# Kernel tuning notes

Measured on AMD Instinct MI355X. Metric: run time of the kernel, lower is better.

Reference implementation:

```python
import jax, jax.numpy as jnp
from jax import lax
import numpy as np

T, B, NIN = 512, 512, 64
H1, H2, H3 = 100, 50, 25


def lstm_layer(x, w_ih, w_hh, b_ih, b_hh):
    # x: [T, B, in]; torch gate order (i, f, g, o); weights [4H, in]/[4H, H]
    H = w_hh.shape[1]
    xg = jnp.einsum('tbi,gi->tbg', x, w_ih) + b_ih + b_hh  # [T, B, 4H]

    def step(carry, xg_t):
        h, c = carry
        g = xg_t + h @ w_hh.T
        i, f, gg, o = jnp.split(g, 4, axis=-1)
        c = jax.nn.sigmoid(f) * c + jax.nn.sigmoid(i) * jnp.tanh(gg)
        h = jax.nn.sigmoid(o) * jnp.tanh(c)
        return (h, c), h

    h0 = jnp.zeros((x.shape[1], H), x.dtype)
    _, hs = lax.scan(step, (h0, h0), xg)
    return hs  # [T, B, H]


def setup_inputs() -> dict:
    key = jax.random.key(0)
    ks = jax.random.split(key, 16)
    s = 0.1  # init scale for stability
    return {
        'x': jax.random.normal(ks[0], (T, B, NIN), jnp.float32),
        'w_ih1': jax.random.normal(ks[1], (4 * H1, NIN), jnp.float32) * s,
        'w_hh1': jax.random.normal(ks[2], (4 * H1, H1), jnp.float32) * s,
        'b_ih1': jax.random.normal(ks[3], (4 * H1,), jnp.float32) * s,
        'b_hh1': jax.random.normal(ks[4], (4 * H1,), jnp.float32) * s,
        'w_ih2': jax.random.normal(ks[5], (4 * H2, H1), jnp.float32) * s,
        'w_hh2': jax.random.normal(ks[6], (4 * H2, H2), jnp.float32) * s,
        'b_ih2': jax.random.normal(ks[7], (4 * H2,), jnp.float32) * s,
        'b_hh2': jax.random.normal(ks[8], (4 * H2,), jnp.float32) * s,
        'w_ih3': jax.random.normal(ks[9], (4 * H3, H2), jnp.float32) * s,
        'w_hh3': jax.random.normal(ks[10], (4 * H3, H3), jnp.float32) * s,
        'b_ih3': jax.random.normal(ks[11], (4 * H3,), jnp.float32) * s,
        'b_hh3': jax.random.normal(ks[12], (4 * H3,), jnp.float32) * s,
        'w_lin': jax.random.normal(ks[13], (1, H3), jnp.float32) * s,
        'b_lin': jax.random.normal(ks[14], (1,), jnp.float32) * s,
    }


def reference(x, w_ih1, w_hh1, b_ih1, b_hh1,
              w_ih2, w_hh2, b_ih2, b_hh2,
              w_ih3, w_hh3, b_ih3, b_hh3,
              w_lin, b_lin):
    # Dropout layers are identity at inference.
    h = lstm_layer(x, w_ih1, w_hh1, b_ih1, b_hh1)
    h = lstm_layer(h, w_ih2, w_hh2, b_ih2, b_hh2)
    h = lstm_layer(h, w_ih3, w_hh3, b_ih3, b_hh3)
    return h @ w_lin.T + b_lin  # [T, B, 1]
```

## Files before the change

### kernel.cpp

```cpp
#include <hip/hip_runtime.h>
#include <math.h>

#define T_STEPS 512
#define BATCH   512

__device__ __forceinline__ float sigmoidf_(float x) {
    return 1.0f / (1.0f + __expf(-x));
}
__device__ __forceinline__ float tanhf_(float x) {
    float ax = fabsf(x);
    float e  = __expf(-2.0f * ax);
    float t  = (1.0f - e) / (1.0f + e);
    return copysignf(t, x);
}
__device__ __forceinline__ float4 ld4(const float* p) {
    return make_float4(p[0], p[1], p[2], p[3]);
}

#define PINF(f)  asm volatile("" : "+v"(f))
#define PIN4(v)  { PINF(v.x); PINF(v.y); PINF(v.z); PINF(v.w); }

__global__ __launch_bounds__(448, 2) void gemm1_kernel(
    const float* __restrict__ A, const float* __restrict__ W,
    const float* __restrict__ bih, const float* __restrict__ bhh,
    float* __restrict__ xg)
{
    __shared__ __align__(16) float As[64 * 64];
    const int tid = threadIdx.x;

    float4 W00,W01,W02,W03,W04,W05,W06,W07,W08,W09,W10,W11,W12,W13,W14,W15;
    float bias = 0.0f;
    if (tid < 400) {
        bias = bih[tid] + bhh[tid];
        const float* wp = W + tid * 64;
        W00=ld4(wp+ 0); W01=ld4(wp+ 4); W02=ld4(wp+ 8); W03=ld4(wp+12);
        W04=ld4(wp+16); W05=ld4(wp+20); W06=ld4(wp+24); W07=ld4(wp+28);
        W08=ld4(wp+32); W09=ld4(wp+36); W10=ld4(wp+40); W11=ld4(wp+44);
        W12=ld4(wp+48); W13=ld4(wp+52); W14=ld4(wp+56); W15=ld4(wp+60);
        PIN4(W00) PIN4(W01) PIN4(W02) PIN4(W03)
        PIN4(W04) PIN4(W05) PIN4(W06) PIN4(W07)
        PIN4(W08) PIN4(W09) PIN4(W10) PIN4(W11)
        PIN4(W12) PIN4(W13) PIN4(W14) PIN4(W15)
        PINF(bias);
    }

    const size_t r0 = (size_t)blockIdx.x * 64;
    const float4* Ag = (const float4*)(A + r0 * 64);
    float4* As4 = (float4*)As;
    for (int i = tid; i < 64 * 16; i += 448) As4[i] = Ag[i];
    __syncthreads();

    if (tid < 400) {
        for (int r = 0; r < 64; ++r) {
            const float4* a4 = (const float4*)(As + r * 64);
            float a0 = bias, a1 = 0.0f;
#define G1V(WV, I) { float4 v = a4[I]; \
            a0 = fmaf(v.x, WV.x, a0); a1 = fmaf(v.y, WV.y, a1); \
            a0 = fmaf(v.z, WV.z, a0); a1 = fmaf(v.w, WV.w, a1); }
            G1V(W00,0) G1V(W01,1) G1V(W02,2) G1V(W03,3)
            G1V(W04,4) G1V(W05,5) G1V(W06,6) G1V(W07,7)
            G1V(W08,8) G1V(W09,9) G1V(W10,10) G1V(W11,11)
            G1V(W12,12) G1V(W13,13) G1V(W14,14) G1V(W15,15)
#undef G1V
            xg[(r0 + r) * 400 + tid] = a0 + a1;
        }
    }
}

__global__ __launch_bounds__(448, 2) void gemm2_kernel(
    const float* __restrict__ A,
    const float* __restrict__ W,
    const float* __restrict__ bih, const float* __restrict__ bhh,
    float* __restrict__ xg)
{
    __shared__ __align__(16) float As[64 * 104];
    __shared__ __align__(16) float ps[8][2][200];

    const int tid  = threadIdx.x;
    const bool slot = (tid < 400);
    const int q = slot ? tid / 200 : 0;
    const int j = slot ? tid % 200 : 0;

    float4 W00,W01,W02,W03,W04,W05,W06,W07,W08,W09,W10,W11,W12;
    float bias = 0.0f;
    if (slot) {
        if (q == 0) bias = bih[j] + bhh[j];
        const float* wp = W + j * 100 + q * 52;
        W00=ld4(wp+ 0); W01=ld4(wp+ 4); W02=ld4(wp+ 8); W03=ld4(wp+12);
        W04=ld4(wp+16); W05=ld4(wp+20); W06=ld4(wp+24); W07=ld4(wp+28);
        W08=ld4(wp+32); W09=ld4(wp+36); W10=ld4(wp+40); W11=ld4(wp+44);
        W12 = q ? make_float4(0.f,0.f,0.f,0.f) : ld4(wp+48);
        PIN4(W00) PIN4(W01) PIN4(W02) PIN4(W03)
        PIN4(W04) PIN4(W05) PIN4(W06) PIN4(W07)
        PIN4(W08) PIN4(W09) PIN4(W10) PIN4(W11)
        PIN4(W12)
        PINF(bias);
    }

    const size_t r0 = (size_t)blockIdx.x * 64;
    const float2* A2 = (const float2*)(A + r0 * 100);
    float2* As2 = (float2*)As;
    for (int i = tid; i < 64 * 50; i += 448) {
        int r = i / 50, k2 = i % 50;
        As2[r * 52 + k2] = A2[i];
    }
    if (tid < 64) {
        As[tid*104+100]=0.f; As[tid*104+101]=0.f;
        As[tid*104+102]=0.f; As[tid*104+103]=0.f;
    }
    __syncthreads();

    const float4* As4 = (const float4*)As;
    const int q13 = q * 13;
    const float base = (q == 0) ? bias : 0.0f;
    for (int g = 0; g < 8; ++g) {
        const int rb = g * 8;
        if (slot) {
#define G2V(P, WV, I) { float4 v = P[I]; \
            A0 = fmaf(v.x, WV.x, A0); A1 = fmaf(v.y, WV.y, A1); \
            A0 = fmaf(v.z, WV.z, A0); A1 = fmaf(v.w, WV.w, A1); }
#define G2ROW(RR) { const float4* a4 = As4 + (rb + RR) * 26 + q13; \
            float A0 = base, A1 = 0.0f; \
            G2V(a4,W00,0) G2V(a4,W01,1) G2V(a4,W02,2) G2V(a4,W03,3) \
            G2V(a4,W04,4) G2V(a4,W05,5) G2V(a4,W06,6) G2V(a4,W07,7) \
            G2V(a4,W08,8) G2V(a4,W09,9) G2V(a4,W10,10) G2V(a4,W11,11) \
            G2V(a4,W12,12) \
            ps[RR][q][j] = A0 + A1; }
            G2ROW(0) G2ROW(1) G2ROW(2) G2ROW(3)
            G2ROW(4) G2ROW(5) G2ROW(6) G2ROW(7)
#undef G2ROW
#undef G2V
        }
        __syncthreads();
        if (tid < 200) {
            #pragma unroll
            for (int rr = 0; rr < 8; ++rr)
                xg[(r0 + rb + rr) * 200 + tid] = ps[rr][0][tid] + ps[rr][1][tid];
        }
        __syncthreads();
    }
}

__global__ __launch_bounds__(832, 3) void scan1_kernel(
    const float* __restrict__ xg,
    const float* __restrict__ w_hh,
    float* __restrict__ h1c,
    float* __restrict__ c1state,
    int t0, int CH)
{
    __shared__ __align__(16) float h_s[2][104];
    __shared__ __align__(16) float ps[2][2][400];

    const int tid   = threadIdx.x;
    const int q     = (tid >= 416) ? 1 : 0;
    const int j     = tid - 416 * q;
    const bool slot = (j < 400);
    const int brow0 = blockIdx.x * 2;

    float4 W00,W01,W02,W03,W04,W05,W06,W07,W08,W09,W10,W11,W12;
    if (slot) {
        const float* wp = w_hh + j * 100 + q * 52;
        W00=ld4(wp+ 0); W01=ld4(wp+ 4); W02=ld4(wp+ 8); W03=ld4(wp+12);
        W04=ld4(wp+16); W05=ld4(wp+20); W06=ld4(wp+24); W07=ld4(wp+28);
        W08=ld4(wp+32); W09=ld4(wp+36); W10=ld4(wp+40); W11=ld4(wp+44);
        W12 = q ? make_float4(0.f,0.f,0.f,0.f) : ld4(wp+48);
        PIN4(W00) PIN4(W01) PIN4(W02) PIN4(W03)
        PIN4(W04) PIN4(W05) PIN4(W06) PIN4(W07)
        PIN4(W08) PIN4(W09) PIN4(W10) PIN4(W11)
        PIN4(W12)
    }

    float c = 0.0f;
    if (tid < 200) {
        int bn = tid / 100, u = tid % 100;
        if (t0 == 0) {
            h_s[bn][u] = 0.0f;
        } else {
            h_s[bn][u] = h1c[((size_t)(CH - 1) * BATCH + brow0 + bn) * 100 + u];
            c          = c1state[(size_t)(brow0 + bn) * 100 + u];
        }
    }
    if (tid >= 200 && tid < 208) {
        int i = tid - 200;
        h_s[i >> 2][100 + (i & 3)] = 0.0f;
    }

    float xgv0 = 0.0f, xgv1 = 0.0f;
    if (slot && q == 0) {
        xgv0 = xg[(size_t)brow0 * 400 + j];
        xgv1 = xg[((size_t)brow0 + 1) * 400 + j];
    }
    __syncthreads();

    const int hq = q * 13;
    for (int tl = 0; tl < CH; ++tl) {
        float pre0 = 0.0f, pre1 = 0.0f;
        if (slot && q == 0 && tl + 1 < CH) {
            pre0 = xg[((size_t)(tl + 1) * BATCH + brow0) * 400 + j];
            pre1 = xg[((size_t)(tl + 1) * BATCH + brow0 + 1) * 400 + j];
        }
        if (slot) {
            const float4* h0 = (const float4*)h_s[0] + hq;
            const float4* h1 = (const float4*)h_s[1] + hq;
            float a00 = xgv0, a01 = 0.0f, a10 = xgv1, a11 = 0.0f;
#define S1ACC(WV, I) { float4 v0 = h0[I], v1 = h1[I]; \
            a00 = fmaf(v0.x, WV.x, a00); a10 = fmaf(v1.x, WV.x, a10); \
            a01 = fmaf(v0.y, WV.y, a01); a11 = fmaf(v1.y, WV.y, a11); \
            a00 = fmaf(v0.z, WV.z, a00); a10 = fmaf(v1.z, WV.z, a10); \
            a01 = fmaf(v0.w, WV.w, a01); a11 = fmaf(v1.w, WV.w, a11); }
            S1ACC(W00,0) S1ACC(W01,1) S1ACC(W02,2) S1ACC(W03,3)
            S1ACC(W04,4) S1ACC(W05,5) S1ACC(W06,6) S1ACC(W07,7)
            S1ACC(W08,8) S1ACC(W09,9) S1ACC(W10,10) S1ACC(W11,11)
            S1ACC(W12,12)
#undef S1ACC
            ps[0][q][j] = a00 + a01;
            ps[1][q][j] = a10 + a11;
        }
        __syncthreads();
        xgv0 = pre0; xgv1 = pre1;
        if (tid < 200) {
            int bn = tid / 100, u = tid % 100;
            float gi = ps[bn][0][u]       + ps[bn][1][u];
            float gf = ps[bn][0][100 + u] + ps[bn][1][100 + u];
            float gg = ps[bn][0][200 + u] + ps[bn][1][200 + u];
            float go = ps[bn][0][300 + u] + ps[bn][1][300 + u];
            c = sigmoidf_(gf) * c + sigmoidf_(gi) * tanhf_(gg);
            float h = sigmoidf_(go) * tanhf_(c);
            h_s[bn][u] = h;
            h1c[((size_t)tl * BATCH + brow0 + bn) * 100 + u] = h;
        }
        __syncthreads();
    }
    if (tid < 200) {
        int bn = tid / 100, u = tid % 100;
        c1state[(size_t)(brow0 + bn) * 100 + u] = c;
    }
}

__global__ __launch_bounds__(384, 2) void scan23_kernel(
    const float* __restrict__ xg2,
    const float* __restrict__ w_hh2,
    const float* __restrict__ w_ih3,
    const float* __restrict__ w_hh3,
    const float* __restrict__ b_ih3, const float* __restrict__ b_hh3,
    const float* __restrict__ w_lin, const float* __restrict__ b_lin,
    float* __restrict__ out,
    float* __restrict__ h2state, float* __restrict__ c2state,
    float* __restrict__ h3state, float* __restrict__ c3state,
    int t0, int CH)
{
    __shared__ __align__(16) float h2_s[52];
    __shared__ __align__(16) float x3_s[2][52];
    __shared__ __align__(16) float h3_s[28];
    __shared__ __align__(16) float h3o_s[2][28];
    __shared__ __align__(16) float g2_s[200];
    __shared__ __align__(16) float g3_s[100];

    const int tid  = threadIdx.x;
    const int brow = blockIdx.x;

    float4 WA0,WA1,WA2,WA3,WA4,WA5,WA6,WA7,WA8,WA9,WA10,WA11,WA12;
    float4 WB0,WB1,WB2,WB3,WB4,WB5,WB6;
    float bias = 0.0f;

#define PINA13 { PIN4(WA0) PIN4(WA1) PIN4(WA2) PIN4(WA3) PIN4(WA4) PIN4(WA5) \
                 PIN4(WA6) PIN4(WA7) PIN4(WA8) PIN4(WA9) PIN4(WA10) PIN4(WA11) \
                 PIN4(WA12) }
#define PINB7  { PIN4(WB0) PIN4(WB1) PIN4(WB2) PIN4(WB3) PIN4(WB4) PIN4(WB5) \
                 PIN4(WB6) }

    if (tid < 200) {
        const float* p = w_hh2 + tid * 50;
        WA0=ld4(p+ 0); WA1=ld4(p+ 4); WA2=ld4(p+ 8); WA3=ld4(p+12);
        WA4=ld4(p+16); WA5=ld4(p+20); WA6=ld4(p+24); WA7=ld4(p+28);
        WA8=ld4(p+32); WA9=ld4(p+36); WA10=ld4(p+40); WA11=ld4(p+44);
        WA12 = make_float4(p[48], p[49], 0.f, 0.f);
        PINA13
    } else if (tid >= 256 && tid < 356) {
        int jj = tid - 256;
        bias = b_ih3[jj] + b_hh3[jj];
        const float* p = w_ih3 + jj * 50;
        WA0=ld4(p+ 0); WA1=ld4(p+ 4); WA2=ld4(p+ 8); WA3=ld4(p+12);
        WA4=ld4(p+16); WA5=ld4(p+20); WA6=ld4(p+24); WA7=ld4(p+28);
        WA8=ld4(p+32); WA9=ld4(p+36); WA10=ld4(p+40); WA11=ld4(p+44);
        WA12 = make_float4(p[48], p[49], 0.f, 0.f);
        const float* p2 = w_hh3 + jj * 25;
        WB0=ld4(p2+ 0); WB1=ld4(p2+ 4); WB2=ld4(p2+ 8);
        WB3=ld4(p2+12); WB4=ld4(p2+16); WB5=ld4(p2+20);
        WB6 = make_float4(p2[24], 0.f, 0.f, 0.f);
        PINA13
        PINB7
        PINF(bias);
    } else if (tid == 370) {
        bias = b_lin[0];
        WA0=ld4(w_lin+ 0); WA1=ld4(w_lin+ 4); WA2=ld4(w_lin+ 8);
        WA3=ld4(w_lin+12); WA4=ld4(w_lin+16); WA5=ld4(w_lin+20);
        WA6 = make_float4(w_lin[24], 0.f, 0.f, 0.f);
        PIN4(WA0) PIN4(WA1) PIN4(WA2) PIN4(WA3) PIN4(WA4) PIN4(WA5) PIN4(WA6)
        PINF(bias);
    }
#undef PINA13
#undef PINB7

    float c2 = 0.0f, c3 = 0.0f;
    if (tid < 52)  { h2_s[tid] = 0.0f; x3_s[0][tid] = 0.0f; x3_s[1][tid] = 0.0f; }
    if (tid >= 52 && tid < 80)  h3_s[tid - 52] = 0.0f;
    if (tid >= 80 && tid < 108) h3o_s[0][tid - 80] = 0.0f;
    if (tid >= 108 && tid < 136) h3o_s[1][tid - 108] = 0.0f;
    __syncthreads();
    if (t0 > 0) {
        if (tid < 50) {
            h2_s[tid] = h2state[(size_t)brow * 50 + tid];
            c2        = c2state[(size_t)brow * 50 + tid];
        }
        if (tid >= 256 && tid < 281) {
            int u = tid - 256;
            h3_s[u] = h3state[(size_t)brow * 25 + u];
            c3      = c3state[(size_t)brow * 25 + u];
        }
    }
    float xgv = (tid < 200) ? xg2[(size_t)brow * 200 + tid] : 0.0f;
    __syncthreads();

    for (int it = 0; it < CH + 2; ++it) {
        float pre = (tid < 200 && it + 1 < CH)
                  ? xg2[((size_t)(it + 1) * BATCH + brow) * 200 + tid] : 0.0f;

        if (tid < 200 && it < CH) {
            const float4* hv = (const float4*)h2_s;
            float a0 = xgv, a1 = 0.0f;
#define SCV(PV, WV, I) { float4 v = PV[I]; \
            a0 = fmaf(v.x, WV.x, a0); a1 = fmaf(v.y, WV.y, a1); \
            a0 = fmaf(v.z, WV.z, a0); a1 = fmaf(v.w, WV.w, a1); }
            SCV(hv,WA0,0) SCV(hv,WA1,1) SCV(hv,WA2,2) SCV(hv,WA3,3)
            SCV(hv,WA4,4) SCV(hv,WA5,5) SCV(hv,WA6,6) SCV(hv,WA7,7)
            SCV(hv,WA8,8) SCV(hv,WA9,9) SCV(hv,WA10,10) SCV(hv,WA11,11)
            SCV(hv,WA12,12)
            g2_s[tid] = a0 + a1;
        }

        if (tid >= 256 && tid < 356 && it >= 1 && it <= CH) {
            const float4* xv = (const float4*)x3_s[(it - 1) & 1];
            const float4* hv = (const float4*)h3_s;
            float a0 = bias, a1 = 0.0f;
            SCV(xv,WA0,0) SCV(xv,WA1,1) SCV(xv,WA2,2) SCV(xv,WA3,3)
            SCV(xv,WA4,4) SCV(xv,WA5,5) SCV(xv,WA6,6) SCV(xv,WA7,7)
            SCV(xv,WA8,8) SCV(xv,WA9,9) SCV(xv,WA10,10) SCV(xv,WA11,11)
            SCV(xv,WA12,12)
            SCV(hv,WB0,0) SCV(hv,WB1,1) SCV(hv,WB2,2) SCV(hv,WB3,3)
            SCV(hv,WB4,4) SCV(hv,WB5,5) SCV(hv,WB6,6)
            g3_s[tid - 256] = a0 + a1;
        }

        if (tid == 370 && it >= 2) {
            const float4* hv = (const float4*)h3o_s[(it - 2) & 1];
            float a0 = bias, a1 = 0.0f;
            SCV(hv,WA0,0) SCV(hv,WA1,1) SCV(hv,WA2,2) SCV(hv,WA3,3)
            SCV(hv,WA4,4) SCV(hv,WA5,5) SCV(hv,WA6,6)
            out[(size_t)(t0 + it - 2) * BATCH + brow] = a0 + a1;
        }
#undef SCV
        __syncthreads();

        if (tid < 200) xgv = pre;

        if (tid < 50 && it < CH) {
            float gi = g2_s[tid],       gf = g2_s[50 + tid];
            float gg = g2_s[100 + tid], go = g2_s[150 + tid];
            c2 = sigmoidf_(gf) * c2 + sigmoidf_(gi) * tanhf_(gg);
            float h = sigmoidf_(go) * tanhf_(c2);
            h2_s[tid] = h;
            x3_s[it & 1][tid] = h;
        }

        if (tid >= 256 && tid < 281 && it >= 1 && it <= CH) {
            int u = tid - 256;
            float gi = g3_s[u],      gf = g3_s[25 + u];
            float gg = g3_s[50 + u], go = g3_s[75 + u];
            c3 = sigmoidf_(gf) * c3 + sigmoidf_(gi) * tanhf_(gg);
            float h = sigmoidf_(go) * tanhf_(c3);
            h3_s[u] = h;
            h3o_s[(it - 1) & 1][u] = h;
        }
        __syncthreads();
    }

    if (tid < 50) {
        h2state[(size_t)brow * 50 + tid] = h2_s[tid];
        c2state[(size_t)brow * 50 + tid] = c2;
    }
    if (tid >= 256 && tid < 281) {
        int u = tid - 256;
        h3state[(size_t)brow * 25 + u] = h3_s[u];
        c3state[(size_t)brow * 25 + u] = c3;
    }
}

extern "C" void kernel_launch(void* const* d_in, const int* in_sizes, int n_in,
                              void* d_out, int out_size, void* d_ws, size_t ws_size,
                              hipStream_t stream)
{
    const float* x     = (const float*)d_in[0];
    const float* w_ih1 = (const float*)d_in[1];
    const float* w_hh1 = (const float*)d_in[2];
    const float* b_ih1 = (const float*)d_in[3];
    const float* b_hh1 = (const float*)d_in[4];
    const float* w_ih2 = (const float*)d_in[5];
    const float* w_hh2 = (const float*)d_in[6];
    const float* b_ih2 = (const float*)d_in[7];
    const float* b_hh2 = (const float*)d_in[8];
    const float* w_ih3 = (const float*)d_in[9];
    const float* w_hh3 = (const float*)d_in[10];
    const float* b_ih3 = (const float*)d_in[11];
    const float* b_hh3 = (const float*)d_in[12];
    const float* w_lin = (const float*)d_in[13];
    const float* b_lin = (const float*)d_in[14];
    float* out = (float*)d_out;

    const size_t state_bytes = (size_t)BATCH * (100 + 50 + 50 + 25 + 25) * sizeof(float);
    int CH = 0;
    for (int c = 128; c >= 8; c >>= 1) {
        size_t need = (size_t)c * BATCH * 700 * sizeof(float) + state_bytes;
        if (need <= ws_size) { CH = c; break; }
    }
    if (CH == 0) return;

    char* ws = (char*)d_ws;
    float* xg1c    = (float*)ws;
    float* h1c     = xg1c + (size_t)CH * BATCH * 400;
    float* xg2c    = h1c  + (size_t)CH * BATCH * 100;
    float* c1state = xg2c + (size_t)CH * BATCH * 200;
    float* h2state = c1state + (size_t)BATCH * 100;
    float* c2state = h2state + (size_t)BATCH * 50;
    float* h3state = c2state + (size_t)BATCH * 50;
    float* c3state = h3state + (size_t)BATCH * 25;

    const int rowtiles = CH * BATCH / 64;

    for (int t0 = 0; t0 < T_STEPS; t0 += CH) {
        gemm1_kernel<<<rowtiles, 448, 0, stream>>>(
            x + (size_t)t0 * BATCH * 64, w_ih1, b_ih1, b_hh1, xg1c);
        scan1_kernel<<<BATCH / 2, 832, 0, stream>>>(xg1c, w_hh1, h1c, c1state, t0, CH);
        gemm2_kernel<<<rowtiles, 448, 0, stream>>>(h1c, w_ih2, b_ih2, b_hh2, xg2c);
        scan23_kernel<<<BATCH, 384, 0, stream>>>(
            xg2c, w_hh2, w_ih3, w_hh3, b_ih3, b_hh3, w_lin, b_lin, out,
            h2state, c2state, h3state, c3state, t0, CH);
    }
}
```

Measured before the change: 1.916 ms.

## Stage layer-1 recurrent weights in LDS and compute all four gates per thread

The layer-1 scan kernel stops holding w_hh in registers split across 832 threads. It now copies the full 400x100 weight matrix into about 160 KB of dynamic LDS, transposed, and each of 200 active threads computes all four gates for one hidden unit of one batch row. This removes the partial-sum exchange through shared memory and the cross-thread gate gather. The cost is reading weights from LDS on every step, staging 160 KB per block, and only one block per CU. The register-pinning asm barriers in the two GEMM kernels are also removed.

```diff
diff --git a/kernel.cpp b/kernel.cpp
--- a/kernel.cpp
+++ b/kernel.cpp
@@ -37,11 +37,6 @@
         W04=ld4(wp+16); W05=ld4(wp+20); W06=ld4(wp+24); W07=ld4(wp+28);
         W08=ld4(wp+32); W09=ld4(wp+36); W10=ld4(wp+40); W11=ld4(wp+44);
         W12=ld4(wp+48); W13=ld4(wp+52); W14=ld4(wp+56); W15=ld4(wp+60);
-        PIN4(W00) PIN4(W01) PIN4(W02) PIN4(W03)
-        PIN4(W04) PIN4(W05) PIN4(W06) PIN4(W07)
-        PIN4(W08) PIN4(W09) PIN4(W10) PIN4(W11)
-        PIN4(W12) PIN4(W13) PIN4(W14) PIN4(W15)
-        PINF(bias);
     }
 
     const size_t r0 = (size_t)blockIdx.x * 64;
@@ -68,8 +63,7 @@
 }
 
 __global__ __launch_bounds__(448, 2) void gemm2_kernel(
-    const float* __restrict__ A,
-    const float* __restrict__ W,
+    const float* __restrict__ A, const float* __restrict__ W,
     const float* __restrict__ bih, const float* __restrict__ bhh,
     float* __restrict__ xg)
 {
@@ -90,11 +84,6 @@
         W04=ld4(wp+16); W05=ld4(wp+20); W06=ld4(wp+24); W07=ld4(wp+28);
         W08=ld4(wp+32); W09=ld4(wp+36); W10=ld4(wp+40); W11=ld4(wp+44);
         W12 = q ? make_float4(0.f,0.f,0.f,0.f) : ld4(wp+48);
-        PIN4(W00) PIN4(W01) PIN4(W02) PIN4(W03)
-        PIN4(W04) PIN4(W05) PIN4(W06) PIN4(W07)
-        PIN4(W08) PIN4(W09) PIN4(W10) PIN4(W11)
-        PIN4(W12)
-        PINF(bias);
     }
 
     const size_t r0 = (size_t)blockIdx.x * 64;
@@ -141,100 +130,85 @@
     }
 }
 
-__global__ __launch_bounds__(832, 3) void scan1_kernel(
+__global__ __launch_bounds__(256, 1) void scan1_kernel(
     const float* __restrict__ xg,
     const float* __restrict__ w_hh,
     float* __restrict__ h1c,
     float* __restrict__ c1state,
     int t0, int CH)
 {
-    __shared__ __align__(16) float h_s[2][104];
-    __shared__ __align__(16) float ps[2][2][400];
-
-    const int tid   = threadIdx.x;
-    const int q     = (tid >= 416) ? 1 : 0;
-    const int j     = tid - 416 * q;
-    const bool slot = (j < 400);
+    extern __shared__ __align__(16) char smem[];
+    float4* wt = (float4*)smem;
+    float* hA = (float*)(smem + 160000);
+    float* hB = (float*)(smem + 160400);
+
+    const int tid = threadIdx.x;
     const int brow0 = blockIdx.x * 2;
 
-    float4 W00,W01,W02,W03,W04,W05,W06,W07,W08,W09,W10,W11,W12;
-    if (slot) {
-        const float* wp = w_hh + j * 100 + q * 52;
-        W00=ld4(wp+ 0); W01=ld4(wp+ 4); W02=ld4(wp+ 8); W03=ld4(wp+12);
-        W04=ld4(wp+16); W05=ld4(wp+20); W06=ld4(wp+24); W07=ld4(wp+28);
-        W08=ld4(wp+32); W09=ld4(wp+36); W10=ld4(wp+40); W11=ld4(wp+44);
-        W12 = q ? make_float4(0.f,0.f,0.f,0.f) : ld4(wp+48);
-        PIN4(W00) PIN4(W01) PIN4(W02) PIN4(W03)
-        PIN4(W04) PIN4(W05) PIN4(W06) PIN4(W07)
-        PIN4(W08) PIN4(W09) PIN4(W10) PIN4(W11)
-        PIN4(W12)
-    }
+    for (int e = tid; e < 10000; e += 256) {
+        int j = e % 400, m = e / 400;
+        wt[m * 400 + j] = *(const float4*)(w_hh + j * 100 + 4 * m);
+    }
+
+    const bool act = (tid < 200);
+    const int u = tid >> 1;
+    const int r = tid & 1;
+    const int row = brow0 + r;
 
     float c = 0.0f;
-    if (tid < 200) {
-        int bn = tid / 100, u = tid % 100;
-        if (t0 == 0) {
-            h_s[bn][u] = 0.0f;
-        } else {
-            h_s[bn][u] = h1c[((size_t)(CH - 1) * BATCH + brow0 + bn) * 100 + u];
-            c          = c1state[(size_t)(brow0 + bn) * 100 + u];
-        }
-    }
-    if (tid >= 200 && tid < 208) {
-        int i = tid - 200;
-        h_s[i >> 2][100 + (i & 3)] = 0.0f;
-    }
-
-    float xgv0 = 0.0f, xgv1 = 0.0f;
-    if (slot && q == 0) {
-        xgv0 = xg[(size_t)brow0 * 400 + j];
-        xgv1 = xg[((size_t)brow0 + 1) * 400 + j];
+    if (act) {
+        float h0 = 0.0f;
+        if (t0 > 0) {
+            h0 = h1c[((size_t)(CH - 1) * BATCH + row) * 100 + u];
+            c  = c1state[(size_t)row * 100 + u];
+        }
+        (r ? hB : hA)[u] = h0;
+    }
+    float xI = 0.f, xF = 0.f, xG = 0.f, xO = 0.f;
+    if (act) {
+        const float* xp = xg + (size_t)row * 400 + u;
+        xI = xp[0]; xF = xp[100]; xG = xp[200]; xO = xp[300];
     }
     __syncthreads();
 
-    const int hq = q * 13;
+    const float4* hr = (const float4*)(r ? hB : hA);
+    float* hw = r ? hB : hA;
+
     for (int tl = 0; tl < CH; ++tl) {
-        float pre0 = 0.0f, pre1 = 0.0f;
-        if (slot && q == 0 && tl + 1 < CH) {
-            pre0 = xg[((size_t)(tl + 1) * BATCH + brow0) * 400 + j];
-            pre1 = xg[((size_t)(tl + 1) * BATCH + brow0 + 1) * 400 + j];
-        }
-        if (slot) {
-            const float4* h0 = (const float4*)h_s[0] + hq;
-            const float4* h1 = (const float4*)h_s[1] + hq;
-            float a00 = xgv0, a01 = 0.0f, a10 = xgv1, a11 = 0.0f;
-#define S1ACC(WV, I) { float4 v0 = h0[I], v1 = h1[I]; \
-            a00 = fmaf(v0.x, WV.x, a00); a10 = fmaf(v1.x, WV.x, a10); \
-            a01 = fmaf(v0.y, WV.y, a01); a11 = fmaf(v1.y, WV.y, a11); \
-            a00 = fmaf(v0.z, WV.z, a00); a10 = fmaf(v1.z, WV.z, a10); \
-            a01 = fmaf(v0.w, WV.w, a01); a11 = fmaf(v1.w, WV.w, a11); }
-            S1ACC(W00,0) S1ACC(W01,1) S1ACC(W02,2) S1ACC(W03,3)
-            S1ACC(W04,4) S1ACC(W05,5) S1ACC(W06,6) S1ACC(W07,7)
-            S1ACC(W08,8) S1ACC(W09,9) S1ACC(W10,10) S1ACC(W11,11)
-            S1ACC(W12,12)
-#undef S1ACC
-            ps[0][q][j] = a00 + a01;
-            ps[1][q][j] = a10 + a11;
-        }
-        __syncthreads();
-        xgv0 = pre0; xgv1 = pre1;
-        if (tid < 200) {
-            int bn = tid / 100, u = tid % 100;
-            float gi = ps[bn][0][u]       + ps[bn][1][u];
-            float gf = ps[bn][0][100 + u] + ps[bn][1][100 + u];
-            float gg = ps[bn][0][200 + u] + ps[bn][1][200 + u];
-            float go = ps[bn][0][300 + u] + ps[bn][1][300 + u];
-            c = sigmoidf_(gf) * c + sigmoidf_(gi) * tanhf_(gg);
-            float h = sigmoidf_(go) * tanhf_(c);
-            h_s[bn][u] = h;
-            h1c[((size_t)tl * BATCH + brow0 + bn) * 100 + u] = h;
-        }
-        __syncthreads();
-    }
-    if (tid < 200) {
-        int bn = tid / 100, u = tid % 100;
-        c1state[(size_t)(brow0 + bn) * 100 + u] = c;
-    }
+        float pI = 0.f, pF = 0.f, pG = 0.f, pO = 0.f;
+        if (act && tl + 1 < CH) {
+            const float* xp = xg + ((size_t)(tl + 1) * BATCH + row) * 400 + u;
+            pI = xp[0]; pF = xp[100]; pG = xp[200]; pO = xp[300];
+        }
+        float aI = xI, aF = xF, aG = xG, aO = xO;
+        if (act) {
+            const float4* wp = wt + u;
+            #pragma unroll
+            for (int m = 0; m < 25; ++m) {
+                float4 hv = hr[m];
+                float4 wi = wp[0], wf = wp[100], wg = wp[200], wo = wp[300];
+                wp += 400;
+                aI = fmaf(hv.x, wi.x, aI); aF = fmaf(hv.x, wf.x, aF);
+                aG = fmaf(hv.x, wg.x, aG); aO = fmaf(hv.x, wo.x, aO);
+                aI = fmaf(hv.y, wi.y, aI); aF = fmaf(hv.y, wf.y, aF);
+                aG = fmaf(hv.y, wg.y, aG); aO = fmaf(hv.y, wo.y, aO);
+                aI = fmaf(hv.z, wi.z, aI); aF = fmaf(hv.z, wf.z, aF);
+                aG = fmaf(hv.z, wg.z, aG); aO = fmaf(hv.z, wo.z, aO);
+                aI = fmaf(hv.w, wi.w, aI); aF = fmaf(hv.w, wf.w, aF);
+                aG = fmaf(hv.w, wg.w, aG); aO = fmaf(hv.w, wo.w, aO);
+            }
+        }
+        __syncthreads();
+        if (act) {
+            c = sigmoidf_(aF) * c + sigmoidf_(aI) * tanhf_(aG);
+            float h = sigmoidf_(aO) * tanhf_(c);
+            hw[u] = h;
+            h1c[((size_t)tl * BATCH + row) * 100 + u] = h;
+            xI = pI; xF = pF; xG = pG; xO = pO;
+        }
+        __syncthreads();
+    }
+    if (act) c1state[(size_t)row * 100 + u] = c;
 }
 
 __global__ __launch_bounds__(384, 2) void scan23_kernel(
@@ -417,6 +391,11 @@
     const float* b_lin = (const float*)d_in[14];
     float* out = (float*)d_out;
 
+    const int SCAN1_LDS = 160000 + 400 + 400;
+    (void)hipFuncSetAttribute((const void*)scan1_kernel,
+                              hipFuncAttributeMaxDynamicSharedMemorySize,
+                              SCAN1_LDS);
+
     const size_t state_bytes = (size_t)BATCH * (100 + 50 + 50 + 25 + 25) * sizeof(float);
     int CH = 0;
     for (int c = 128; c >= 8; c >>= 1) {
@@ -440,7 +419,8 @@
     for (int t0 = 0; t0 < T_STEPS; t0 += CH) {
         gemm1_kernel<<<rowtiles, 448, 0, stream>>>(
             x + (size_t)t0 * BATCH * 64, w_ih1, b_ih1, b_hh1, xg1c);
-        scan1_kernel<<<BATCH / 2, 832, 0, stream>>>(xg1c, w_hh1, h1c, c1state, t0, CH);
+        scan1_kernel<<<BATCH / 2, 256, SCAN1_LDS, stream>>>(
+            xg1c, w_hh1, h1c, c1state, t0, CH);
         gemm2_kernel<<<rowtiles, 448, 0, stream>>>(h1c, w_ih2, b_ih2, b_hh2, xg2c);
         scan23_kernel<<<BATCH, 384, 0, stream>>>(
             xg2c, w_hh2, w_ih3, w_hh3, b_ih3, b_hh3, w_lin, b_lin, out,
```

After: 2.624 ms. 1.37x slower.
